# Kernel optimization log

Hardware: AMD Instinct MI355X
Metric: run time of the kernel (lower is better)

Reference implementation:

```python
import jax, jax.numpy as jnp
import numpy as np

HEAD = 16
EMB = 1024
D_K = EMB // HEAD


def setup_inputs() -> dict:
    key = jax.random.key(0)
    ks = jax.random.split(key, 11)
    B, S, E = 2, 2048, EMB
    scale = 1.0 / np.sqrt(E)
    inp = {
        "query": jax.random.normal(ks[0], (B, S, E), jnp.float32),
        "key": jax.random.normal(ks[1], (B, S, E), jnp.float32),
        "value": jax.random.normal(ks[2], (B, S, E), jnp.float32),
        "Wq": jax.random.normal(ks[3], (E, E), jnp.float32) * scale,
        "bq": jnp.zeros((E,), jnp.float32),
        "Wk": jax.random.normal(ks[4], (E, E), jnp.float32) * scale,
        "bk": jnp.zeros((E,), jnp.float32),
        "Wv": jax.random.normal(ks[5], (E, E), jnp.float32) * scale,
        "bv": jnp.zeros((E,), jnp.float32),
        "Wo": jax.random.normal(ks[6], (E, E), jnp.float32) * scale,
        "bo": jnp.zeros((E,), jnp.float32),
    }
    return inp


def reference(query, key, value, Wq, bq, Wk, bk, Wv, bv, Wo, bo):
    B, S, E = query.shape
    # 3 input projections, split into heads: [B, H, S, d_k]
    def proj(x, W, b):
        return (x @ W.T + b).reshape(B, S, HEAD, D_K).transpose(0, 2, 1, 3)

    q = proj(query, Wq, bq)
    k = proj(key, Wk, bk)
    v = proj(value, Wv, bv)

    # scaled dot-product attention (full matrix, as in original)
    scores = jnp.einsum("bhqd,bhkd->bhqk", q, k) / jnp.sqrt(jnp.float32(D_K))
    attn = jax.nn.softmax(scores, axis=-1)  # dropout in eval mode = identity
    x = jnp.einsum("bhqk,bhkd->bhqd", attn, v)

    # merge heads and output projection
    x = x.transpose(0, 2, 1, 3).reshape(B, S, E)
    return x @ Wo.T + bo
```

## Files before the change

### kernel.cpp

```cpp
#include <hip/hip_runtime.h>
#include <hip/hip_bf16.h>
#include <math.h>


constexpr int Sn = 2048;
constexpr int En = 1024;
constexpr int Hn = 16;
constexpr int Dk = 64;
constexpr int Kn = 1024;
constexpr size_t WSZ = 1048576;
constexpr size_t TSZ = 4194304;
constexpr int PST = 72;

typedef __bf16 bf16x8 __attribute__((ext_vector_type(8)));
typedef float  f32x4  __attribute__((ext_vector_type(4)));

union U16 { uint4 u; bf16x8 v; __hip_bfloat16 h[8]; };
union U8  { uint2 u; __hip_bfloat162 h2[2]; __hip_bfloat16 h[4]; };

__device__ inline U16 cvt8f(const float* __restrict__ p) {
    float4 a = *(const float4*)p;
    float4 b = *(const float4*)(p + 4);
    U16 r;
    r.h[0] = __float2bfloat16(a.x); r.h[1] = __float2bfloat16(a.y);
    r.h[2] = __float2bfloat16(a.z); r.h[3] = __float2bfloat16(a.w);
    r.h[4] = __float2bfloat16(b.x); r.h[5] = __float2bfloat16(b.y);
    r.h[6] = __float2bfloat16(b.z); r.h[7] = __float2bfloat16(b.w);
    return r;
}

__device__ inline void gload16(const __hip_bfloat16* g, __hip_bfloat16* l) {
    __builtin_amdgcn_global_load_lds(
        (const __attribute__((address_space(1))) void*)g,
        (__attribute__((address_space(3))) void*)l, 16, 0, 0);
}

template<int ROWS, int NW>
__device__ inline void stage_tile(const __hip_bfloat16* __restrict__ src, int ld,
                                  __hip_bfloat16* lds, int w, int lane) {
    int l8 = lane >> 3;
    int g = (lane & 7) ^ (l8 & 7);
    #pragma unroll
    for (int j = 0; j < ROWS / (8 * NW); ++j) {
        int c = j * NW + w;
        gload16(src + (size_t)(c * 8 + l8) * ld + g * 8, lds + c * 512);
    }
}

__global__ __launch_bounds__(256)
void cvt_w(const float* __restrict__ w0, const float* __restrict__ w1,
           const float* __restrict__ w2, const float* __restrict__ w3,
           __hip_bfloat16* __restrict__ dst)
{
    int y = blockIdx.y;
    const float* src = (y == 0) ? w0 : (y == 1) ? w1 : (y == 2) ? w2 : w3;
    size_t i = ((size_t)blockIdx.x * 256 + threadIdx.x) * 8;
    U16 r = cvt8f(src + i);
    *(uint4*)&dst[(size_t)y * WSZ + i] = r.u;
}

__global__ __launch_bounds__(256)
void cvt_x(const float* __restrict__ src, __hip_bfloat16* __restrict__ dst)
{
    size_t i = ((size_t)blockIdx.x * 256 + threadIdx.x) * 8;
    U16 r = cvt8f(src + i);
    *(uint4*)&dst[i] = r.u;
}

template<int MODE>
__global__ __launch_bounds__(256)
void gemm64(const __hip_bfloat16* __restrict__ A, const __hip_bfloat16* __restrict__ W,
            const float* __restrict__ bias, void* __restrict__ outp)
{
    __shared__ __align__(16) __hip_bfloat16 As[64 * 64];
    __shared__ __align__(16) __hip_bfloat16 Bs[128 * 64];

    const int tid = threadIdx.x, w = tid >> 6, lane = tid & 63;
    const int l15 = lane & 15, lg = lane >> 4, l7 = lane & 7;
    const int blockM = blockIdx.x * 64, blockN = blockIdx.y * 128;
    const int wm = (w & 1) * 32, wn = (w >> 1) * 64;
    const int coff0 = (lg ^ l7) * 8;
    const int coff1 = ((4 + lg) ^ l7) * 8;

    f32x4 acc[2][4];
    #pragma unroll
    for (int i = 0; i < 2; ++i)
        #pragma unroll
        for (int j = 0; j < 4; ++j) acc[i][j] = {0.f, 0.f, 0.f, 0.f};

    for (int k0 = 0; k0 < Kn; k0 += 64) {
        stage_tile<64, 4>(A + (size_t)blockM * Kn + k0, Kn, As, w, lane);
        stage_tile<128, 4>(W + (size_t)blockN * Kn + k0, Kn, Bs, w, lane);
        __syncthreads();

        U16 af[2][2], bf[4][2];
        #pragma unroll
        for (int mt = 0; mt < 2; ++mt) {
            int r = (wm + mt * 16 + l15) * 64;
            af[mt][0].u = *(const uint4*)&As[r + coff0];
            af[mt][1].u = *(const uint4*)&As[r + coff1];
        }
        #pragma unroll
        for (int nt = 0; nt < 4; ++nt) {
            int r = (wn + nt * 16 + l15) * 64;
            bf[nt][0].u = *(const uint4*)&Bs[r + coff0];
            bf[nt][1].u = *(const uint4*)&Bs[r + coff1];
        }
        #pragma unroll
        for (int mt = 0; mt < 2; ++mt)
            #pragma unroll
            for (int nt = 0; nt < 4; ++nt) {
                acc[mt][nt] = __builtin_amdgcn_mfma_f32_16x16x32_bf16(af[mt][0].v, bf[nt][0].v, acc[mt][nt], 0, 0, 0);
                acc[mt][nt] = __builtin_amdgcn_mfma_f32_16x16x32_bf16(af[mt][1].v, bf[nt][1].v, acc[mt][nt], 0, 0, 0);
            }
        __syncthreads();
    }

    #pragma unroll
    for (int nt = 0; nt < 4; ++nt) {
        int n = blockN + wn + nt * 16 + l15;
        float bvn = bias[n];
        int h_ = n >> 6, d_ = n & 63;
        #pragma unroll
        for (int mt = 0; mt < 2; ++mt) {
            int m0 = blockM + wm + mt * 16 + lg * 4;
            if constexpr (MODE == 0) {
                float* out = (float*)outp;
                #pragma unroll
                for (int i = 0; i < 4; ++i)
                    out[(size_t)(m0 + i) * Kn + n] = acc[mt][nt][i] + bvn;
            } else if constexpr (MODE == 1) {
                __hip_bfloat16* out = (__hip_bfloat16*)outp;
                int b_ = m0 >> 11, s_ = m0 & (Sn - 1);
                #pragma unroll
                for (int i = 0; i < 4; ++i)
                    out[(((size_t)b_ * Hn + h_) * Sn + s_ + i) * Dk + d_] =
                        __float2bfloat16(acc[mt][nt][i] + bvn);
            } else {
                __hip_bfloat16* out = (__hip_bfloat16*)outp;
                int b_ = m0 >> 11, s_ = m0 & (Sn - 1);
                U8 pk;
                #pragma unroll
                for (int i = 0; i < 4; ++i) pk.h[i] = __float2bfloat16(acc[mt][nt][i] + bvn);
                *(uint2*)&out[(((size_t)b_ * Hn + h_) * Dk + d_) * Sn + s_] = pk.u;
            }
        }
    }
}

__global__ __launch_bounds__(256)
void attn(const __hip_bfloat16* __restrict__ Q, const __hip_bfloat16* __restrict__ K,
          const __hip_bfloat16* __restrict__ Vt, __hip_bfloat16* __restrict__ X)
{
    __shared__ __align__(16) __hip_bfloat16 Ks[2][64 * 64];
    __shared__ __align__(16) __hip_bfloat16 Vts[2][64 * 64];
    __shared__ __align__(16) __hip_bfloat16 Ps[128 * PST];

    const int bh = blockIdx.y, q0 = blockIdx.x * 128;
    const int tid = threadIdx.x, w = tid >> 6, lane = tid & 63;
    const int l15 = lane & 15, lg = lane >> 4, l7 = lane & 7;
    const int coff0 = (lg ^ l7) * 8;
    const int coff1 = ((4 + lg) ^ l7) * 8;

    const __hip_bfloat16* Qb = Q  + (size_t)bh * Sn * Dk;
    const __hip_bfloat16* Kb = K  + (size_t)bh * Sn * Dk;
    const __hip_bfloat16* Vb = Vt + (size_t)bh * Dk * Sn;

    U16 aq[2][2];
    #pragma unroll
    for (int qt = 0; qt < 2; ++qt) {
        const __hip_bfloat16* qp = Qb + (size_t)(q0 + w * 32 + qt * 16 + l15) * Dk + lg * 8;
        aq[qt][0].u = *(const uint4*)qp;
        aq[qt][1].u = *(const uint4*)(qp + 32);
    }

    f32x4 o[2][4];
    float lpart[2];
    #pragma unroll
    for (int qt = 0; qt < 2; ++qt) {
        lpart[qt] = 0.f;
        #pragma unroll
        for (int dt = 0; dt < 4; ++dt) o[qt][dt] = {0.f, 0.f, 0.f, 0.f};
    }

    __hip_bfloat16* Pw = Ps + (w * 32) * PST;

    stage_tile<64, 4>(Kb, Dk, Ks[0], w, lane);
    stage_tile<64, 4>(Vb, Sn, Vts[0], w, lane);

    for (int t = 0; t < Sn / 64; ++t) {
        __syncthreads();
        const int cur = t & 1;
        if (t + 1 < Sn / 64) {
            stage_tile<64, 4>(Kb + (size_t)(t + 1) * 64 * Dk, Dk, Ks[cur ^ 1], w, lane);
            stage_tile<64, 4>(Vb + (t + 1) * 64, Sn, Vts[cur ^ 1], w, lane);
        }

        U16 kf[4][2];
        #pragma unroll
        for (int kt = 0; kt < 4; ++kt) {
            int r = (kt * 16 + l15) * 64;
            kf[kt][0].u = *(const uint4*)&Ks[cur][r + coff0];
            kf[kt][1].u = *(const uint4*)&Ks[cur][r + coff1];
        }
        #pragma unroll
        for (int kt = 0; kt < 4; ++kt)
            #pragma unroll
            for (int qt = 0; qt < 2; ++qt) {
                f32x4 s = {0.f, 0.f, 0.f, 0.f};
                s = __builtin_amdgcn_mfma_f32_16x16x32_bf16(kf[kt][0].v, aq[qt][0].v, s, 0, 0, 0);
                s = __builtin_amdgcn_mfma_f32_16x16x32_bf16(kf[kt][1].v, aq[qt][1].v, s, 0, 0, 0);
                float p0 = __expf(s[0] * 0.125f), p1 = __expf(s[1] * 0.125f);
                float p2 = __expf(s[2] * 0.125f), p3 = __expf(s[3] * 0.125f);
                lpart[qt] += (p0 + p1) + (p2 + p3);
                U8 pk;
                pk.h2[0] = __float22bfloat162_rn({p0, p1});
                pk.h2[1] = __float22bfloat162_rn({p2, p3});
                *(uint2*)&Pw[(qt * 16 + l15) * PST + kt * 16 + lg * 4] = pk.u;
            }

        U16 pf[2][2], vf[4][2];
        #pragma unroll
        for (int qt = 0; qt < 2; ++qt) {
            const __hip_bfloat16* pr = &Pw[(qt * 16 + l15) * PST + lg * 8];
            pf[qt][0].u = *(const uint4*)pr;
            pf[qt][1].u = *(const uint4*)(pr + 32);
        }
        #pragma unroll
        for (int dt = 0; dt < 4; ++dt) {
            int r = (dt * 16 + l15) * 64;
            vf[dt][0].u = *(const uint4*)&Vts[cur][r + coff0];
            vf[dt][1].u = *(const uint4*)&Vts[cur][r + coff1];
        }
        #pragma unroll
        for (int qt = 0; qt < 2; ++qt)
            #pragma unroll
            for (int dt = 0; dt < 4; ++dt) {
                o[qt][dt] = __builtin_amdgcn_mfma_f32_16x16x32_bf16(pf[qt][0].v, vf[dt][0].v, o[qt][dt], 0, 0, 0);
                o[qt][dt] = __builtin_amdgcn_mfma_f32_16x16x32_bf16(pf[qt][1].v, vf[dt][1].v, o[qt][dt], 0, 0, 0);
            }
    }

    float linv[2][4];
    #pragma unroll
    for (int qt = 0; qt < 2; ++qt) {
        float v = lpart[qt];
        v += __shfl_xor(v, 16, 64);
        v += __shfl_xor(v, 32, 64);
        #pragma unroll
        for (int i = 0; i < 4; ++i)
            linv[qt][i] = 1.f / __shfl(v, lg * 4 + i, 16);
    }

    int b_ = bh >> 4, h_ = bh & (Hn - 1);
    #pragma unroll
    for (int qt = 0; qt < 2; ++qt)
        #pragma unroll
        for (int i = 0; i < 4; ++i) {
            int sr = q0 + w * 32 + qt * 16 + lg * 4 + i;
            __hip_bfloat16* xp = X + ((size_t)(b_ * Sn + sr)) * En + h_ * Dk + l15;
            #pragma unroll
            for (int dt = 0; dt < 4; ++dt)
                xp[dt * 16] = __float2bfloat16(o[qt][dt][i] * linv[qt][i]);
        }
}

extern "C" void kernel_launch(void* const* d_in, const int* in_sizes, int n_in,
                              void* d_out, int out_size, void* d_ws, size_t ws_size,
                              hipStream_t stream)
{
    const float* query = (const float*)d_in[0];
    const float* key   = (const float*)d_in[1];
    const float* value = (const float*)d_in[2];
    const float* Wq = (const float*)d_in[3];
    const float* bq = (const float*)d_in[4];
    const float* Wk = (const float*)d_in[5];
    const float* bk = (const float*)d_in[6];
    const float* Wv = (const float*)d_in[7];
    const float* bv = (const float*)d_in[8];
    const float* Wo = (const float*)d_in[9];
    const float* bo = (const float*)d_in[10];
    float* out = (float*)d_out;

    __hip_bfloat16* xbuf = (__hip_bfloat16*)d_ws;
    __hip_bfloat16* Wbf  = xbuf + TSZ;
    __hip_bfloat16* Qw   = Wbf + 4 * WSZ;
    __hip_bfloat16* Kw   = Qw + TSZ;
    __hip_bfloat16* Vtw  = Kw + TSZ;
    __hip_bfloat16* Xw   = xbuf;

    dim3 ggrid(64, 8);

    cvt_w<<<dim3(512, 4), 256, 0, stream>>>(Wq, Wk, Wv, Wo, Wbf);
    cvt_x<<<2048, 256, 0, stream>>>(query, xbuf);
    gemm64<1><<<ggrid, 256, 0, stream>>>(xbuf, Wbf, bq, Qw);
    cvt_x<<<2048, 256, 0, stream>>>(key, xbuf);
    gemm64<1><<<ggrid, 256, 0, stream>>>(xbuf, Wbf + WSZ, bk, Kw);
    cvt_x<<<2048, 256, 0, stream>>>(value, xbuf);
    gemm64<2><<<ggrid, 256, 0, stream>>>(xbuf, Wbf + 2 * WSZ, bv, Vtw);
    attn<<<dim3(Sn / 128, 32), 256, 0, stream>>>(Qw, Kw, Vtw, Xw);
    gemm64<0><<<ggrid, 256, 0, stream>>>(Xw, Wbf + 3 * WSZ, bo, out);
}
```

Measured before the change: 245.1 us.

## Batch QKV conversion and projections into single launches, fold softmax scale into Q

The three input conversions and three projection GEMMs are merged into one launch each, using a z grid dimension, so each launch fills the GPU with more blocks and there are fewer kernel boundaries. The softmax scale and log2(e) are folded into the Q projection epilogue, so attention can use a raw exp2 instead of a multiply plus expf. The output GEMM uses 64x64 tiles to double its block count for better occupancy. This needs a larger workspace to hold three converted inputs at once, and the Q values are stored pre-scaled in bf16.

```diff
diff --git a/kernel.cpp b/kernel.cpp
--- a/kernel.cpp
+++ b/kernel.cpp
@@ -11,6 +11,8 @@
 constexpr size_t WSZ = 1048576;
 constexpr size_t TSZ = 4194304;
 constexpr int PST = 72;
+
+#define QSCALE 0.18033688011112042f
 
 typedef __bf16 bf16x8 __attribute__((ext_vector_type(8)));
 typedef float  f32x4  __attribute__((ext_vector_type(4)));
@@ -60,40 +62,38 @@
 }
 
 __global__ __launch_bounds__(256)
-void cvt_x(const float* __restrict__ src, __hip_bfloat16* __restrict__ dst)
-{
+void cvt_x3(const float* __restrict__ q, const float* __restrict__ k,
+            const float* __restrict__ v, __hip_bfloat16* __restrict__ dst)
+{
+    int z = blockIdx.y;
+    const float* src = (z == 0) ? q : (z == 1) ? k : v;
     size_t i = ((size_t)blockIdx.x * 256 + threadIdx.x) * 8;
     U16 r = cvt8f(src + i);
-    *(uint4*)&dst[i] = r.u;
-}
-
-template<int MODE>
-__global__ __launch_bounds__(256)
-void gemm64(const __hip_bfloat16* __restrict__ A, const __hip_bfloat16* __restrict__ W,
-            const float* __restrict__ bias, void* __restrict__ outp)
-{
-    __shared__ __align__(16) __hip_bfloat16 As[64 * 64];
-    __shared__ __align__(16) __hip_bfloat16 Bs[128 * 64];
-
-    const int tid = threadIdx.x, w = tid >> 6, lane = tid & 63;
+    *(uint4*)&dst[(size_t)z * TSZ + i] = r.u;
+}
+
+template<int NT>
+__device__ inline void gemm_core(const __hip_bfloat16* __restrict__ Ab,
+                                 const __hip_bfloat16* __restrict__ Wb,
+                                 __hip_bfloat16* As, __hip_bfloat16* Bs,
+                                 f32x4 (&acc)[2][NT], int w, int lane)
+{
     const int l15 = lane & 15, lg = lane >> 4, l7 = lane & 7;
-    const int blockM = blockIdx.x * 64, blockN = blockIdx.y * 128;
-    const int wm = (w & 1) * 32, wn = (w >> 1) * 64;
+    const int wm = (w & 1) * 32, wn = (w >> 1) * (NT * 16);
     const int coff0 = (lg ^ l7) * 8;
     const int coff1 = ((4 + lg) ^ l7) * 8;
 
-    f32x4 acc[2][4];
     #pragma unroll
     for (int i = 0; i < 2; ++i)
         #pragma unroll
-        for (int j = 0; j < 4; ++j) acc[i][j] = {0.f, 0.f, 0.f, 0.f};
+        for (int j = 0; j < NT; ++j) acc[i][j] = {0.f, 0.f, 0.f, 0.f};
 
     for (int k0 = 0; k0 < Kn; k0 += 64) {
-        stage_tile<64, 4>(A + (size_t)blockM * Kn + k0, Kn, As, w, lane);
-        stage_tile<128, 4>(W + (size_t)blockN * Kn + k0, Kn, Bs, w, lane);
+        stage_tile<64, 4>(Ab + k0, Kn, As, w, lane);
+        stage_tile<NT * 32, 4>(Wb + k0, Kn, Bs, w, lane);
         __syncthreads();
 
-        U16 af[2][2], bf[4][2];
+        U16 af[2][2], bf[NT][2];
         #pragma unroll
         for (int mt = 0; mt < 2; ++mt) {
             int r = (wm + mt * 16 + l15) * 64;
@@ -101,7 +101,7 @@
             af[mt][1].u = *(const uint4*)&As[r + coff1];
         }
         #pragma unroll
-        for (int nt = 0; nt < 4; ++nt) {
+        for (int nt = 0; nt < NT; ++nt) {
             int r = (wn + nt * 16 + l15) * 64;
             bf[nt][0].u = *(const uint4*)&Bs[r + coff0];
             bf[nt][1].u = *(const uint4*)&Bs[r + coff1];
@@ -109,41 +109,90 @@
         #pragma unroll
         for (int mt = 0; mt < 2; ++mt)
             #pragma unroll
-            for (int nt = 0; nt < 4; ++nt) {
+            for (int nt = 0; nt < NT; ++nt) {
                 acc[mt][nt] = __builtin_amdgcn_mfma_f32_16x16x32_bf16(af[mt][0].v, bf[nt][0].v, acc[mt][nt], 0, 0, 0);
                 acc[mt][nt] = __builtin_amdgcn_mfma_f32_16x16x32_bf16(af[mt][1].v, bf[nt][1].v, acc[mt][nt], 0, 0, 0);
             }
         __syncthreads();
     }
+}
+
+__global__ __launch_bounds__(256)
+void gemm_qkv(const __hip_bfloat16* __restrict__ X, const __hip_bfloat16* __restrict__ Wall,
+              const float* __restrict__ bq, const float* __restrict__ bk,
+              const float* __restrict__ bv, __hip_bfloat16* __restrict__ outbase)
+{
+    __shared__ __align__(16) __hip_bfloat16 As[64 * 64];
+    __shared__ __align__(16) __hip_bfloat16 Bs[128 * 64];
+
+    const int tid = threadIdx.x, w = tid >> 6, lane = tid & 63;
+    const int z = blockIdx.z;
+    const int blockM = blockIdx.x * 64, blockN = blockIdx.y * 128;
+
+    f32x4 acc[2][4];
+    gemm_core<4>(X + (size_t)z * TSZ + (size_t)blockM * Kn,
+                 Wall + (size_t)z * WSZ + (size_t)blockN * Kn,
+                 As, Bs, acc, w, lane);
+
+    const float scale = (z == 0) ? QSCALE : 1.0f;
+    const float* bias = (z == 0) ? bq : (z == 1) ? bk : bv;
+    __hip_bfloat16* out = outbase + (size_t)z * TSZ;
+
+    const int l15 = lane & 15, lg = lane >> 4;
+    const int wm = (w & 1) * 32, wn = (w >> 1) * 64;
 
     #pragma unroll
     for (int nt = 0; nt < 4; ++nt) {
         int n = blockN + wn + nt * 16 + l15;
-        float bvn = bias[n];
+        float bvn = bias[n] * scale;
         int h_ = n >> 6, d_ = n & 63;
         #pragma unroll
         for (int mt = 0; mt < 2; ++mt) {
             int m0 = blockM + wm + mt * 16 + lg * 4;
-            if constexpr (MODE == 0) {
-                float* out = (float*)outp;
-                #pragma unroll
-                for (int i = 0; i < 4; ++i)
-                    out[(size_t)(m0 + i) * Kn + n] = acc[mt][nt][i] + bvn;
-            } else if constexpr (MODE == 1) {
-                __hip_bfloat16* out = (__hip_bfloat16*)outp;
-                int b_ = m0 >> 11, s_ = m0 & (Sn - 1);
+            int b_ = m0 >> 11, s_ = m0 & (Sn - 1);
+            if (z < 2) {
                 #pragma unroll
                 for (int i = 0; i < 4; ++i)
                     out[(((size_t)b_ * Hn + h_) * Sn + s_ + i) * Dk + d_] =
-                        __float2bfloat16(acc[mt][nt][i] + bvn);
+                        __float2bfloat16(fmaf(acc[mt][nt][i], scale, bvn));
             } else {
-                __hip_bfloat16* out = (__hip_bfloat16*)outp;
-                int b_ = m0 >> 11, s_ = m0 & (Sn - 1);
                 U8 pk;
                 #pragma unroll
-                for (int i = 0; i < 4; ++i) pk.h[i] = __float2bfloat16(acc[mt][nt][i] + bvn);
+                for (int i = 0; i < 4; ++i)
+                    pk.h[i] = __float2bfloat16(fmaf(acc[mt][nt][i], scale, bvn));
                 *(uint2*)&out[(((size_t)b_ * Hn + h_) * Dk + d_) * Sn + s_] = pk.u;
             }
+        }
+    }
+}
+
+__global__ __launch_bounds__(256)
+void gemm_out(const __hip_bfloat16* __restrict__ A, const __hip_bfloat16* __restrict__ W,
+              const float* __restrict__ bias, float* __restrict__ out)
+{
+    __shared__ __align__(16) __hip_bfloat16 As[64 * 64];
+    __shared__ __align__(16) __hip_bfloat16 Bs[64 * 64];
+
+    const int tid = threadIdx.x, w = tid >> 6, lane = tid & 63;
+    const int blockM = blockIdx.x * 64, blockN = blockIdx.y * 64;
+
+    f32x4 acc[2][2];
+    gemm_core<2>(A + (size_t)blockM * Kn, W + (size_t)blockN * Kn,
+                 As, Bs, acc, w, lane);
+
+    const int l15 = lane & 15, lg = lane >> 4;
+    const int wm = (w & 1) * 32, wn = (w >> 1) * 32;
+
+    #pragma unroll
+    for (int nt = 0; nt < 2; ++nt) {
+        int n = blockN + wn + nt * 16 + l15;
+        float bvn = bias[n];
+        #pragma unroll
+        for (int mt = 0; mt < 2; ++mt) {
+            int m0 = blockM + wm + mt * 16 + lg * 4;
+            #pragma unroll
+            for (int i = 0; i < 4; ++i)
+                out[(size_t)(m0 + i) * Kn + n] = acc[mt][nt][i] + bvn;
         }
     }
 }
@@ -210,8 +259,8 @@
                 f32x4 s = {0.f, 0.f, 0.f, 0.f};
                 s = __builtin_amdgcn_mfma_f32_16x16x32_bf16(kf[kt][0].v, aq[qt][0].v, s, 0, 0, 0);
                 s = __builtin_amdgcn_mfma_f32_16x16x32_bf16(kf[kt][1].v, aq[qt][1].v, s, 0, 0, 0);
-                float p0 = __expf(s[0] * 0.125f), p1 = __expf(s[1] * 0.125f);
-                float p2 = __expf(s[2] * 0.125f), p3 = __expf(s[3] * 0.125f);
+                float p0 = __builtin_amdgcn_exp2f(s[0]), p1 = __builtin_amdgcn_exp2f(s[1]);
+                float p2 = __builtin_amdgcn_exp2f(s[2]), p3 = __builtin_amdgcn_exp2f(s[3]);
                 lpart[qt] += (p0 + p1) + (p2 + p3);
                 U8 pk;
                 pk.h2[0] = __float22bfloat162_rn({p0, p1});
@@ -282,22 +331,14 @@
     const float* bo = (const float*)d_in[10];
     float* out = (float*)d_out;
 
-    __hip_bfloat16* xbuf = (__hip_bfloat16*)d_ws;
-    __hip_bfloat16* Wbf  = xbuf + TSZ;
-    __hip_bfloat16* Qw   = Wbf + 4 * WSZ;
-    __hip_bfloat16* Kw   = Qw + TSZ;
-    __hip_bfloat16* Vtw  = Kw + TSZ;
-    __hip_bfloat16* Xw   = xbuf;
-
-    dim3 ggrid(64, 8);
+    __hip_bfloat16* xqkv = (__hip_bfloat16*)d_ws;
+    __hip_bfloat16* Wbf  = xqkv + 3 * TSZ;
+    __hip_bfloat16* QKVw = Wbf + 4 * WSZ;
+    __hip_bfloat16* Xw   = xqkv;
 
     cvt_w<<<dim3(512, 4), 256, 0, stream>>>(Wq, Wk, Wv, Wo, Wbf);
-    cvt_x<<<2048, 256, 0, stream>>>(query, xbuf);
-    gemm64<1><<<ggrid, 256, 0, stream>>>(xbuf, Wbf, bq, Qw);
-    cvt_x<<<2048, 256, 0, stream>>>(key, xbuf);
-    gemm64<1><<<ggrid, 256, 0, stream>>>(xbuf, Wbf + WSZ, bk, Kw);
-    cvt_x<<<2048, 256, 0, stream>>>(value, xbuf);
-    gemm64<2><<<ggrid, 256, 0, stream>>>(xbuf, Wbf + 2 * WSZ, bv, Vtw);
-    attn<<<dim3(Sn / 128, 32), 256, 0, stream>>>(Qw, Kw, Vtw, Xw);
-    gemm64<0><<<ggrid, 256, 0, stream>>>(Xw, Wbf + 3 * WSZ, bo, out);
-}
+    cvt_x3<<<dim3(2048, 3), 256, 0, stream>>>(query, key, value, xqkv);
+    gemm_qkv<<<dim3(64, 8, 3), 256, 0, stream>>>(xqkv, Wbf, bq, bk, bv, QKVw);
+    attn<<<dim3(Sn / 128, 32), 256, 0, stream>>>(QKVw, QKVw + TSZ, QKVw + 2 * TSZ, Xw);
+    gemm_out<<<dim3(64, 16), 256, 0, stream>>>(Xw, Wbf + 3 * WSZ, bo, out);
+}
```

Measured after the change: 222.8 us. 9.1% less time.
